# Kernel tuning notes

Measured on AMD Instinct MI355X. Metric: run time of the kernel, lower is better.

Reference implementation:

```python
import jax, jax.numpy as jnp
import numpy as np

N_NODES = 110000   # users + items per domain
NUM_USER = 60000   # item offset
ALPHA = 1.0        # gradient-reversal scale (identity in forward)


def _gcn(x, src, dst, W, b):
    # PyG GCNConv: x@W, add self-loops, symmetric D^-1/2 (A+I) D^-1/2, +bias
    xw = x @ W
    sl = jnp.arange(N_NODES)
    s = jnp.concatenate([src, sl])
    d = jnp.concatenate([dst, sl])
    deg = jax.ops.segment_sum(jnp.ones(d.shape[0], xw.dtype), d, num_segments=N_NODES)
    dinv = jnp.where(deg > 0, jax.lax.rsqrt(deg), 0.0)
    msg = xw[s] * (dinv[s] * dinv[d])[:, None]
    return jax.ops.segment_sum(msg, d, num_segments=N_NODES) + b


def _bce(p, y):
    # torch BCELoss (mean, log clamped at -100)
    lp = jnp.clip(jnp.log(p), -100.0)
    lq = jnp.clip(jnp.log(1.0 - p), -100.0)
    return -jnp.mean(y * lp + (1.0 - y) * lq)


def setup_inputs():
    key = jax.random.key(0)
    ks = jax.random.split(key, 22)
    F_IN, H, E, B = 128, 128, 1600000, 100000
    inp = {}
    inp['feats_s'] = jax.random.normal(ks[0], (N_NODES, F_IN), jnp.float32)
    inp['feats_t'] = jax.random.normal(ks[1], (N_NODES, F_IN), jnp.float32)
    inp['adj_ds'] = jax.random.randint(ks[2], (2, E), 0, N_NODES)
    inp['adj_dt'] = jax.random.randint(ks[3], (2, E), 0, N_NODES)
    inp['user_s'] = jax.random.randint(ks[4], (B,), 0, NUM_USER)
    inp['item_s'] = jax.random.randint(ks[5], (B,), 0, N_NODES - NUM_USER)
    inp['labels_s'] = jax.random.randint(ks[6], (B,), 0, 2)
    inp['user_t'] = jax.random.randint(ks[7], (B,), 0, NUM_USER)
    inp['item_t'] = jax.random.randint(ks[8], (B,), 0, N_NODES - NUM_USER)
    inp['labels_t'] = jax.random.randint(ks[9], (B,), 0, 2)
    SH = 2 * H  # sum(hidden_dims)
    inp['W1'] = jax.random.normal(ks[10], (F_IN, H), jnp.float32) / np.sqrt(F_IN)
    inp['b1'] = jnp.zeros((H,), jnp.float32)
    inp['W2'] = jax.random.normal(ks[11], (H, H), jnp.float32) / np.sqrt(H)
    inp['b2'] = jnp.zeros((H,), jnp.float32)
    inp['Wp'] = jax.random.normal(ks[12], (2 * SH, 1), jnp.float32) / np.sqrt(2 * SH)
    inp['bp'] = jnp.zeros((1,), jnp.float32)
    inp['Wdu'] = jax.random.normal(ks[13], (SH, 1), jnp.float32) / np.sqrt(SH)
    inp['bdu'] = jnp.zeros((1,), jnp.float32)
    inp['Wdi'] = jax.random.normal(ks[14], (SH, 1), jnp.float32) / np.sqrt(SH)
    inp['bdi'] = jnp.zeros((1,), jnp.float32)
    return inp


def reference(feats_s, feats_t, adj_ds, adj_dt, user_s, item_s, labels_s,
              user_t, item_t, labels_t, W1, b1, W2, b2, Wp, bp, Wdu, bdu, Wdi, bdi):
    x_ds, x_dt = feats_s, feats_t
    uf_s, if_s, uf_t, if_t = [], [], [], []
    for (W, b) in ((W1, b1), (W2, b2)):
        x_ds = jax.nn.relu(_gcn(x_ds, adj_ds[0], adj_ds[1], W, b))
        x_dt = jax.nn.relu(_gcn(x_dt, adj_dt[0], adj_dt[1], W, b))
        uf_s.append(x_ds[user_s]); if_s.append(x_ds[item_s + NUM_USER])
        uf_t.append(x_dt[user_t]); if_t.append(x_dt[item_t + NUM_USER])
    uf_s = jnp.concatenate(uf_s, axis=1); if_s = jnp.concatenate(if_s, axis=1)
    uf_t = jnp.concatenate(uf_t, axis=1); if_t = jnp.concatenate(if_t, axis=1)
    p_s = jax.nn.sigmoid(jnp.concatenate([uf_s, if_s], 1) @ Wp + bp).reshape(-1)
    p_t = jax.nn.sigmoid(jnp.concatenate([uf_t, if_t], 1) @ Wp + bp).reshape(-1)
    loss = _bce(p_s, labels_s.astype(jnp.float32)) + _bce(p_t, labels_t.astype(jnp.float32))
    # gradient reversal is identity in forward
    pu = jax.nn.sigmoid(jnp.concatenate([uf_s, uf_t], 0) @ Wdu + bdu).reshape(-1)
    pi = jax.nn.sigmoid(jnp.concatenate([if_s, if_t], 0) @ Wdi + bdi).reshape(-1)
    B = uf_s.shape[0]
    dlab = jnp.concatenate([jnp.zeros((B,), jnp.float32), jnp.ones((uf_t.shape[0],), jnp.float32)])
    domain_loss = _bce(pi, dlab) + _bce(pu, dlab)
    return loss + domain_loss * 0.1
```

## Files before the change

kernel.cpp:

```cpp
#include <hip/hip_runtime.h>

#define N_NODES 110000
#define NUM_USER 60000
#define MPAD 110080
#define ZROW N_NODES
#define BSHIFT 9
#define NBUCK 256
#define NPB 512
#define EPB 8192
#define SCAP 9216

typedef __attribute__((ext_vector_type(8))) __bf16 bf16x8;
typedef __attribute__((ext_vector_type(4))) float f32x4;
typedef __attribute__((ext_vector_type(2))) float f32x2;
typedef __attribute__((ext_vector_type(4))) unsigned int uint4v;

union UB { uint4v u; bf16x8 b; };

__device__ __forceinline__ unsigned short f2b(float f) {
    unsigned int u = __float_as_uint(f);
    unsigned int r = (u + 0x7FFFu + ((u >> 16) & 1u)) >> 16;
    return (unsigned short)r;
}
__device__ __forceinline__ float b2f(unsigned short h) {
    return __uint_as_float(((unsigned int)h) << 16);
}
__device__ __forceinline__ unsigned f2e4m3(float x) {
    unsigned u = __float_as_uint(x * 0x1p-120f);
    unsigned r = u + 0x7FFFFu + ((u >> 20) & 1u);
    return ((r >> 20) & 0x7Fu) | ((u >> 24) & 0x80u);
}
__device__ __forceinline__ float e4m3f(unsigned v) {
    unsigned bits = ((v & 0x80u) << 24) | ((v & 0x7Fu) << 20);
    return __uint_as_float(bits) * 0x1p+120f;
}


__global__ __launch_bounds__(256) void init_k(const float* __restrict__ W1, const float* __restrict__ W2,
        ushort* __restrict__ W1h, ushort* __restrict__ W1l,
        ushort* __restrict__ W2h, ushort* __restrict__ W2l,
        unsigned char* __restrict__ Tp0, unsigned char* __restrict__ Tp1,
        float* __restrict__ acc, int* __restrict__ bcnt) {
    int b = blockIdx.x, tid = threadIdx.x;
    if (b < 128) {
        const float* W = (b < 64) ? W1 : W2;
        ushort* hi = (b < 64) ? W1h : W2h;
        ushort* lo = (b < 64) ? W1l : W2l;
        int i = (b & 63) * 256 + tid;
        int k = i >> 7, n = i & 127;
        float w = W[i];
        ushort h = f2b(w);
        hi[(n << 7) | k] = h;
        lo[(n << 7) | k] = f2b(w - b2f(h));
    } else if (b < 130) {
        unsigned char* Tp = (b == 128) ? Tp0 : Tp1;
        for (int j = tid; j < (MPAD - N_NODES) * 128; j += 256)
            Tp[(size_t)N_NODES * 128 + j] = 0;
    } else {
        if (tid < 16) acc[tid] = 0.f;
        bcnt[tid] = 0;
        bcnt[256 + tid] = 0;
    }
}


__global__ __launch_bounds__(256) void bin2_k(const int* __restrict__ adj0, const int* __restrict__ adj1,
        int* __restrict__ bcnt, unsigned int* __restrict__ stg, int E, int nbE) {
    __shared__ int h[NBUCK];
    __shared__ int lcur[NBUCK];
    int b = blockIdx.x, tid = threadIdx.x;
    int dom = b / nbE, blk = b - dom * nbE;
    const int* src = (dom ? adj1 : adj0);
    const int* dst = src + E;
    unsigned int* sg = stg + (size_t)dom * NBUCK * SCAP;
    h[tid] = 0;
    __syncthreads();
    int base = blk * EPB, end = min(base + EPB, E);
    for (int i = base + tid * 4; i + 3 < end; i += 1024) {
        int4 d = *(const int4*)&dst[i];
        atomicAdd(&h[d.x >> BSHIFT], 1); atomicAdd(&h[d.y >> BSHIFT], 1);
        atomicAdd(&h[d.z >> BSHIFT], 1); atomicAdd(&h[d.w >> BSHIFT], 1);
    }
    __syncthreads();
    lcur[tid] = tid * SCAP + atomicAdd(&bcnt[dom * NBUCK + tid], h[tid]);
    __syncthreads();
    for (int i = base + tid * 4; i + 3 < end; i += 1024) {
        int4 s = *(const int4*)&src[i];
        int4 d = *(const int4*)&dst[i];
        int p;
        p = atomicAdd(&lcur[d.x >> BSHIFT], 1); sg[p] = (unsigned)s.x | ((unsigned)(d.x & (NPB - 1)) << 17);
        p = atomicAdd(&lcur[d.y >> BSHIFT], 1); sg[p] = (unsigned)s.y | ((unsigned)(d.y & (NPB - 1)) << 17);
        p = atomicAdd(&lcur[d.z >> BSHIFT], 1); sg[p] = (unsigned)s.z | ((unsigned)(d.z & (NPB - 1)) << 17);
        p = atomicAdd(&lcur[d.w >> BSHIFT], 1); sg[p] = (unsigned)s.w | ((unsigned)(d.w & (NPB - 1)) << 17);
    }
}

__global__ __launch_bounds__(256) void csr_k(const unsigned int* __restrict__ stg,
        const int* __restrict__ bcnt,
        int* __restrict__ deg, float* __restrict__ dinv, int* __restrict__ off,
        int* __restrict__ idxb, int N, int nbB) {
    __shared__ int ldeg[NPB];
    __shared__ int lcur[NPB];
    __shared__ int shp[256];
    __shared__ unsigned int lidx[SCAP];
    int b = blockIdx.x, tid = threadIdx.x;
    int dom = b / nbB, blk = b - dom * nbB;
    const unsigned int* sg = stg + ((size_t)dom * NBUCK + blk) * SCAP;
    int* degd = deg + (size_t)dom * N_NODES;
    float* dinvd = dinv + (size_t)dom * N_NODES;
    int* offd = off + (size_t)dom * N_NODES;
    int* idxd = idxb + (size_t)dom * NBUCK * SCAP;
    int node0 = blk * NPB;
    int base = blk * SCAP;
    int cnt = bcnt[dom * NBUCK + blk];
    ldeg[tid] = 0; ldeg[tid + 256] = 0;
    __syncthreads();
    for (int i = tid; i < cnt; i += 256)
        atomicAdd(&ldeg[sg[i] >> 17], 1);
    __syncthreads();
    int a0 = ldeg[2 * tid], a1 = ldeg[2 * tid + 1];
    shp[tid] = a0 + a1;
    __syncthreads();
    for (int o = 1; o < 256; o <<= 1) {
        int v = (tid >= o) ? shp[tid - o] : 0;
        __syncthreads();
        shp[tid] += v;
        __syncthreads();
    }
    int excl = shp[tid] - a0 - a1;
    lcur[2 * tid] = excl;
    lcur[2 * tid + 1] = excl + a0;
    int n0 = node0 + 2 * tid;
    if (n0 < N)     { degd[n0] = a0;     dinvd[n0] = rsqrtf(a0 + 1.f);     offd[n0] = base + excl; }
    if (n0 + 1 < N) { degd[n0 + 1] = a1; dinvd[n0 + 1] = rsqrtf(a1 + 1.f); offd[n0 + 1] = base + excl + a0; }
    __syncthreads();
    for (int i = tid; i < cnt; i += 256) {
        unsigned e = sg[i];
        int p = atomicAdd(&lcur[e >> 17], 1);
        if (p < SCAP) lidx[p] = e & 0x1FFFFu;
    }
    __syncthreads();
    for (int i = tid; i < cnt; i += 256)
        idxd[base + i] = (int)lidx[i];
}


template<bool F32A>
__global__ __launch_bounds__(256) void mm_k(const float* __restrict__ Xf0, const float* __restrict__ Xf1,
        const ushort* __restrict__ Xhi0, const ushort* __restrict__ Xhi1,
        const ushort* __restrict__ Whi, const ushort* __restrict__ Wlo,
        const float* __restrict__ dinv2, unsigned char* __restrict__ Tp0, unsigned char* __restrict__ Tp1,
        int M, int gHalf) {
    __shared__ ushort ldsW[2][1024 * 8];
    int bid = blockIdx.x;
    int dom = bid >= gHalf;
    bid -= dom * gHalf;
    const float* Xf = dom ? Xf1 : Xf0;
    const ushort* Xhi = dom ? Xhi1 : Xhi0;
    const float* dinv = dinv2 + (size_t)dom * N_NODES;
    unsigned char* Tp = dom ? Tp1 : Tp0;
    int tid = threadIdx.x;
    int wid = tid >> 6, lane = tid & 63;
    int l15 = lane & 15;
    int kg = (lane >> 4) * 8;
    int row0 = bid * 128 + wid * 32;
    int rA0 = row0 + l15;
    int rA1 = row0 + 16 + l15;
    f32x4 acc[2][8] = {};
    #pragma unroll
    for (int ph = 0; ph < 2; ph++) {
        if (ph) __syncthreads();
        #pragma unroll
        for (int i = 0; i < 8; i++) {
            int arr = i >> 2;
            int f = tid + (i & 3) * 256;
            int l = f & 63;
            int nr = ((f >> 6) & 7) * 16 + (l & 15);
            int kc = (2 * ph + (f >> 9)) * 32 + (l >> 4) * 8;
            const ushort* srcp = (arr ? Wlo : Whi) + nr * 128 + kc;
            *(uint4v*)&ldsW[arr][(size_t)f * 8] = *(const uint4v*)srcp;
        }
        __syncthreads();
        #pragma unroll
        for (int gg = 0; gg < 2; gg++) {
            int g = 2 * ph + gg;
            int k0 = g * 32 + kg;
            UB a0hi, a0lo, a1hi, a1lo;
            if (F32A) {
                #pragma unroll
                for (int s = 0; s < 2; s++) {
                    int rA = s ? rA1 : rA0;
                    float4 f0 = make_float4(0.f, 0.f, 0.f, 0.f), f1 = f0;
                    if (rA < M) {
                        f0 = *(const float4*)&Xf[(size_t)rA * 128 + k0];
                        f1 = *(const float4*)&Xf[(size_t)rA * 128 + k0 + 4];
                    }
                    float fv[8] = {f0.x, f0.y, f0.z, f0.w, f1.x, f1.y, f1.z, f1.w};
                    ushort h[8], l[8];
                    #pragma unroll
                    for (int j = 0; j < 8; j++) { h[j] = f2b(fv[j]); l[j] = f2b(fv[j] - b2f(h[j])); }
                    uint4v hu = uint4v{(uint)h[0] | ((uint)h[1] << 16), (uint)h[2] | ((uint)h[3] << 16),
                                       (uint)h[4] | ((uint)h[5] << 16), (uint)h[6] | ((uint)h[7] << 16)};
                    uint4v lu = uint4v{(uint)l[0] | ((uint)l[1] << 16), (uint)l[2] | ((uint)l[3] << 16),
                                       (uint)l[4] | ((uint)l[5] << 16), (uint)l[6] | ((uint)l[7] << 16)};
                    if (s) { a1hi.u = hu; a1lo.u = lu; } else { a0hi.u = hu; a0lo.u = lu; }
                }
            } else {
                a0hi.u = *(const uint4v*)&Xhi[(size_t)rA0 * 128 + k0];
                a1hi.u = *(const uint4v*)&Xhi[(size_t)rA1 * 128 + k0];
            }
            #pragma unroll
            for (int n = 0; n < 8; n++) {
                int fbase = ((gg * 8 + n) * 64 + lane) * 8;
                UB bhi, blo;
                bhi.u = *(const uint4v*)&ldsW[0][fbase];
                blo.u = *(const uint4v*)&ldsW[1][fbase];
                acc[0][n] = __builtin_amdgcn_mfma_f32_16x16x32_bf16(a0hi.b, bhi.b, acc[0][n], 0, 0, 0);
                acc[0][n] = __builtin_amdgcn_mfma_f32_16x16x32_bf16(a0hi.b, blo.b, acc[0][n], 0, 0, 0);
                if (F32A)
                    acc[0][n] = __builtin_amdgcn_mfma_f32_16x16x32_bf16(a0lo.b, bhi.b, acc[0][n], 0, 0, 0);
                acc[1][n] = __builtin_amdgcn_mfma_f32_16x16x32_bf16(a1hi.b, bhi.b, acc[1][n], 0, 0, 0);
                acc[1][n] = __builtin_amdgcn_mfma_f32_16x16x32_bf16(a1hi.b, blo.b, acc[1][n], 0, 0, 0);
                if (F32A)
                    acc[1][n] = __builtin_amdgcn_mfma_f32_16x16x32_bf16(a1lo.b, bhi.b, acc[1][n], 0, 0, 0);
            }
        }
    }
    #pragma unroll
    for (int s = 0; s < 2; s++) {
        int rbase = row0 + s * 16 + (lane >> 4) * 4;
        #pragma unroll
        for (int r = 0; r < 4; r++) {
            int row = rbase + r;
            if (row < M) {
                float dv = dinv[row];
                #pragma unroll
                for (int n = 0; n < 8; n++)
                    Tp[(size_t)row * 128 + n * 16 + l15] = (unsigned char)f2e4m3(dv * acc[s][n][r]);
            }
        }
    }
}


template<bool STORE_F>
__global__ __launch_bounds__(256) void aggregate_k(
        const unsigned char* __restrict__ Tp0, const unsigned char* __restrict__ Tp1,
        const int* __restrict__ idxb, const int* __restrict__ off, const int* __restrict__ deg,
        const float* __restrict__ dinv2, const float* __restrict__ bias,
        const float* __restrict__ Wp, const float* __restrict__ Wdu, const float* __restrict__ Wdi,
        int loff, float* __restrict__ nd0, float* __restrict__ nd1,
        ushort* __restrict__ ohi0, ushort* __restrict__ ohi1, int N, int gHalf) {
    int bid = blockIdx.x;
    int dom = bid >= gHalf;
    bid -= dom * gHalf;
    const unsigned char* Tp = dom ? Tp1 : Tp0;
    const int* idxd = idxb + (size_t)dom * NBUCK * SCAP;
    const int* offd = off + (size_t)dom * N_NODES;
    const int* degd = deg + (size_t)dom * N_NODES;
    const float* dinv = dinv2 + (size_t)dom * N_NODES;
    float* nd = dom ? nd1 : nd0;
    ushort* ohi = dom ? ohi1 : ohi0;

    int w = threadIdx.x >> 6, lane = threadIdx.x & 63;
    int d = bid * 4 + w;
    int grp = lane >> 4, li = lane & 15;
    int db = li * 8;
    if (d >= N) {
        if (STORE_F && grp == 0) *(uint4*)&ohi[(size_t)d * 128 + db] = make_uint4(0, 0, 0, 0);
        return;
    }
    f32x2 A0 = {0.f, 0.f}, A1 = {0.f, 0.f}, A2 = {0.f, 0.f}, A3 = {0.f, 0.f};
    int o = offd[d];
    int cnt = degd[d] + 1;
    unsigned laneoff = (unsigned)(li << 3);
    for (int c = 0; c < cnt; c += 64) {
        int p = c + lane;
        int id = ZROW;
        if (p < cnt) id = (p == 0) ? d : idxd[o + p - 1];
        int m = min(64, cnt - c);
        #pragma unroll 4
        for (int jj = 0; jj * 4 < m; jj++) {
            int s = __shfl(id, jj * 4 + grp);
            uint2 u = *(const uint2*)(Tp + (((unsigned)s << 7) | laneoff));
#if __has_builtin(__builtin_amdgcn_cvt_pk_f32_fp8)
            A0 += __builtin_amdgcn_cvt_pk_f32_fp8(u.x, false);
            A1 += __builtin_amdgcn_cvt_pk_f32_fp8(u.x, true);
            A2 += __builtin_amdgcn_cvt_pk_f32_fp8(u.y, false);
            A3 += __builtin_amdgcn_cvt_pk_f32_fp8(u.y, true);
#else
            A0 += f32x2{e4m3f(u.x & 0xFF),         e4m3f((u.x >> 8) & 0xFF)};
            A1 += f32x2{e4m3f((u.x >> 16) & 0xFF), e4m3f(u.x >> 24)};
            A2 += f32x2{e4m3f(u.y & 0xFF),         e4m3f((u.y >> 8) & 0xFF)};
            A3 += f32x2{e4m3f((u.y >> 16) & 0xFF), e4m3f(u.y >> 24)};
#endif
        }
    }
    float a0 = A0[0], a1 = A0[1], a2 = A1[0], a3 = A1[1];
    float a4 = A2[0], a5 = A2[1], a6 = A3[0], a7 = A3[1];
    #define RED2(x) { x += __shfl_xor(x, 16); x += __shfl_xor(x, 32); }
    RED2(a0) RED2(a1) RED2(a2) RED2(a3) RED2(a4) RED2(a5) RED2(a6) RED2(a7)
    #undef RED2
    float di = dinv[d];
    float4 b0 = *(const float4*)&bias[db];
    float4 b1 = *(const float4*)&bias[db + 4];
    float f0 = fmaxf(di * a0 + b0.x, 0.f);
    float f1 = fmaxf(di * a1 + b0.y, 0.f);
    float f2 = fmaxf(di * a2 + b0.z, 0.f);
    float f3 = fmaxf(di * a3 + b0.w, 0.f);
    float f4 = fmaxf(di * a4 + b1.x, 0.f);
    float f5 = fmaxf(di * a5 + b1.y, 0.f);
    float f6 = fmaxf(di * a6 + b1.z, 0.f);
    float f7 = fmaxf(di * a7 + b1.w, 0.f);
    if (STORE_F && grp == 0) {
        ushort h0 = f2b(f0), h1 = f2b(f1), h2 = f2b(f2), h3 = f2b(f3);
        ushort h4 = f2b(f4), h5 = f2b(f5), h6 = f2b(f6), h7 = f2b(f7);
        uint4 hv = make_uint4((uint)h0 | ((uint)h1 << 16), (uint)h2 | ((uint)h3 << 16),
                              (uint)h4 | ((uint)h5 << 16), (uint)h6 | ((uint)h7 << 16));
        *(uint4*)&ohi[(size_t)d * 128 + db] = hv;
    }
    const float* wsel = (grp == 0) ? Wp + loff : (grp == 1) ? Wp + 256 + loff
                      : (grp == 2) ? Wdu + loff : Wdi + loff;
    float4 w0 = *(const float4*)&wsel[db];
    float4 w1 = *(const float4*)&wsel[db + 4];
    float dt = f0 * w0.x + f1 * w0.y + f2 * w0.z + f3 * w0.w
             + f4 * w1.x + f5 * w1.y + f6 * w1.z + f7 * w1.w;
    dt += __shfl_xor(dt, 1); dt += __shfl_xor(dt, 2);
    dt += __shfl_xor(dt, 4); dt += __shfl_xor(dt, 8);
    if (li == 0) nd[(size_t)d * 4 + grp] = dt;
}


__device__ __forceinline__ float sp100(float z) {
    float sp = (z > 0.f) ? (z + log1pf(expf(-z))) : log1pf(expf(z));
    return fminf(sp, 100.f);
}
__device__ __forceinline__ float wred64(float x) {
    #pragma unroll
    for (int o = 32; o > 0; o >>= 1) x += __shfl_xor(x, o);
    return x;
}

__global__ __launch_bounds__(256) void loss_k(
        const float4* __restrict__ nd1_0, const float4* __restrict__ nd1_1,
        const float4* __restrict__ nd2_0, const float4* __restrict__ nd2_1,
        const int* __restrict__ user0, const int* __restrict__ user1,
        const int* __restrict__ item0, const int* __restrict__ item1,
        const int* __restrict__ lab0, const int* __restrict__ lab1,
        const float* __restrict__ bp, const float* __restrict__ bdu, const float* __restrict__ bdi,
        float* __restrict__ acc, int B, int gHalf) {
    __shared__ float sh[3][4];
    int bid = blockIdx.x;
    int dom = bid >= gHalf;
    bid -= dom * gHalf;
    const float4* nd1 = dom ? nd1_1 : nd1_0;
    const float4* nd2 = dom ? nd2_1 : nd2_0;
    const int* user = dom ? user1 : user0;
    const int* item = dom ? item1 : item0;
    const int* labels = dom ? lab1 : lab0;
    int gtid = bid * blockDim.x + threadIdx.x;
    int nth = gHalf * blockDim.x;
    float bpv = bp[0], bduv = bdu[0], bdiv = bdi[0];
    float lp = 0.f, lu = 0.f, li = 0.f;
    for (int s = gtid; s < B; s += nth) {
        int u = user[s];
        int it = item[s] + NUM_USER;
        float4 a = nd1[u], b = nd2[u], c = nd1[it], dd = nd2[it];
        float zp = a.x + b.x + c.y + dd.y + bpv;
        float zu = a.z + b.z + bduv;
        float zi = c.w + dd.w + bdiv;
        lp += labels[s] ? sp100(-zp) : sp100(zp);
        lu += dom ? sp100(-zu) : sp100(zu);
        li += dom ? sp100(-zi) : sp100(zi);
    }
    lp = wred64(lp); lu = wred64(lu); li = wred64(li);
    int lane = threadIdx.x & 63, w = threadIdx.x >> 6;
    if (lane == 0) { sh[0][w] = lp; sh[1][w] = lu; sh[2][w] = li; }
    __syncthreads();
    if (threadIdx.x == 0) {
        float s0 = 0.f, s1 = 0.f, s2 = 0.f;
        for (int j = 0; j < 4; j++) { s0 += sh[0][j]; s1 += sh[1][j]; s2 += sh[2][j]; }
        atomicAdd(&acc[dom], s0);
        atomicAdd(&acc[2], s1);
        atomicAdd(&acc[3], s2);
    }
}

__global__ void fin_k(const float* __restrict__ acc, float* __restrict__ out, int B) {
    float invB = 1.f / (float)B;
    out[0] = acc[0] * invB + acc[1] * invB + 0.1f * ((acc[2] + acc[3]) * (0.5f * invB));
}


extern "C" void kernel_launch(void* const* d_in, const int* in_sizes, int n_in,
                              void* d_out, int out_size, void* d_ws, size_t ws_size,
                              hipStream_t stream) {
    const float* feats[2] = {(const float*)d_in[0], (const float*)d_in[1]};
    const int* adj[2]    = {(const int*)d_in[2], (const int*)d_in[3]};
    const int* user[2]   = {(const int*)d_in[4], (const int*)d_in[7]};
    const int* item[2]   = {(const int*)d_in[5], (const int*)d_in[8]};
    const int* labels[2] = {(const int*)d_in[6], (const int*)d_in[9]};
    const float* Wl[2] = {(const float*)d_in[10], (const float*)d_in[12]};
    const float* bl[2] = {(const float*)d_in[11], (const float*)d_in[13]};
    const float* Wp  = (const float*)d_in[14];
    const float* bp  = (const float*)d_in[15];
    const float* Wdu = (const float*)d_in[16];
    const float* bdu = (const float*)d_in[17];
    const float* Wdi = (const float*)d_in[18];
    const float* bdi = (const float*)d_in[19];

    const int E = in_sizes[2] / 2;
    const int B = in_sizes[4];
    const int N = N_NODES;

    char* w = (char*)d_ws;
    unsigned char* Tp0 = (unsigned char*)w; w += (size_t)MPAD * 128;
    unsigned char* Tp1 = (unsigned char*)w; w += (size_t)MPAD * 128;
    ushort* Fhi0 = (ushort*)w; w += (size_t)MPAD * 128 * 2;
    ushort* Fhi1 = (ushort*)w; w += (size_t)MPAD * 128 * 2;
    ushort* W1h  = (ushort*)w; w += 16384 * 2;
    ushort* W1l  = (ushort*)w; w += 16384 * 2;
    ushort* W2h  = (ushort*)w; w += 16384 * 2;
    ushort* W2l  = (ushort*)w; w += 16384 * 2;
    float* nd1_0 = (float*)w; w += (size_t)MPAD * 16;
    float* nd1_1 = (float*)w; w += (size_t)MPAD * 16;
    float* nd2_0 = (float*)w; w += (size_t)MPAD * 16;
    float* nd2_1 = (float*)w; w += (size_t)MPAD * 16;
    int*   deg  = (int*)w;   w += (size_t)2 * N * 4;
    float* dinv = (float*)w; w += (size_t)2 * N * 4;
    int*   off  = (int*)w;   w += (size_t)2 * N * 4;
    int*   idxb = (int*)w;   w += (size_t)2 * NBUCK * SCAP * 4;
    unsigned int* stg = (unsigned int*)w; w += (size_t)2 * NBUCK * SCAP * 4;
    int*   bcnt = (int*)w;   w += 2 * NBUCK * 4;
    float* acc  = (float*)w; w += 64;

    int nbE = (E + EPB - 1) / EPB;
    int nbB = (N + NPB - 1) / NPB;
    int gMM = MPAD / 128;
    int gAG = MPAD / 4;

    init_k<<<131, 256, 0, stream>>>(Wl[0], Wl[1], W1h, W1l, W2h, W2l, Tp0, Tp1, acc, bcnt);

    bin2_k<<<2 * nbE, 256, 0, stream>>>(adj[0], adj[1], bcnt, stg, E, nbE);
    csr_k<<<2 * nbB, 256, 0, stream>>>(stg, bcnt, deg, dinv, off, idxb, N, nbB);

    mm_k<true><<<2 * gMM, 256, 0, stream>>>(feats[0], feats[1], nullptr, nullptr,
                                            W1h, W1l, dinv, Tp0, Tp1, N, gMM);
    aggregate_k<true><<<2 * gAG, 256, 0, stream>>>(Tp0, Tp1, idxb, off, deg, dinv, bl[0],
                                                   Wp, Wdu, Wdi, 0, nd1_0, nd1_1, Fhi0, Fhi1, N, gAG);
    mm_k<false><<<2 * gMM, 256, 0, stream>>>(nullptr, nullptr, Fhi0, Fhi1,
                                             W2h, W2l, dinv, Tp0, Tp1, N, gMM);
    aggregate_k<false><<<2 * gAG, 256, 0, stream>>>(Tp0, Tp1, idxb, off, deg, dinv, bl[1],
                                                    Wp, Wdu, Wdi, 128, nd2_0, nd2_1, nullptr, nullptr, N, gAG);

    loss_k<<<256, 256, 0, stream>>>((const float4*)nd1_0, (const float4*)nd1_1,
                                    (const float4*)nd2_0, (const float4*)nd2_1,
                                    user[0], user[1], item[0], item[1], labels[0], labels[1],
                                    bp, bdu, bdi, acc, B, 128);
    fin_k<<<1, 1, 0, stream>>>(acc, (float*)d_out, B);
}
```

Before: 406.5 us.

## Process two destination nodes per wavefront in GCN aggregation

The aggregation kernel now assigns two destination nodes per 64-lane wavefront (one per 32-lane half) instead of one, each half split into two 16-lane groups that gather alternate neighbors. Neighbor indices are loaded directly per iteration rather than staged and shuffled, and the projection dot-products compute two outputs per group. The grid is halved accordingly. This aims to cut idle lanes and loop overhead for the low average degree (~15 neighbors), but the two halves iterate to the larger of their counts, so divergence can waste work when degrees differ.

```diff
diff --git a/kernel.cpp b/kernel.cpp
--- a/kernel.cpp
+++ b/kernel.cpp
@@ -263,26 +263,31 @@
     ushort* ohi = dom ? ohi1 : ohi0;
 
     int w = threadIdx.x >> 6, lane = threadIdx.x & 63;
-    int d = bid * 4 + w;
-    int grp = lane >> 4, li = lane & 15;
+    int half = lane >> 5;
+    int grp = (lane >> 4) & 1;
+    int li = lane & 15;
+    int d = bid * 8 + w * 2 + half;
     int db = li * 8;
-    if (d >= N) {
+    bool valid = d < N;
+    int o = 0, cnt = 0;
+    if (valid) { o = offd[d]; cnt = degd[d] + 1; }
+    int cmax = max(cnt, __shfl_xor(cnt, 32));
+    if (!valid) {
         if (STORE_F && grp == 0) *(uint4*)&ohi[(size_t)d * 128 + db] = make_uint4(0, 0, 0, 0);
         return;
     }
     f32x2 A0 = {0.f, 0.f}, A1 = {0.f, 0.f}, A2 = {0.f, 0.f}, A3 = {0.f, 0.f};
-    int o = offd[d];
-    int cnt = degd[d] + 1;
     unsigned laneoff = (unsigned)(li << 3);
-    for (int c = 0; c < cnt; c += 64) {
-        int p = c + lane;
-        int id = ZROW;
-        if (p < cnt) id = (p == 0) ? d : idxd[o + p - 1];
-        int m = min(64, cnt - c);
+    int ob = o + grp - 1;
+    for (int c = 0; c < cmax; c += 32) {
+        int m = min(32, cmax - c);
         #pragma unroll 4
-        for (int jj = 0; jj * 4 < m; jj++) {
-            int s = __shfl(id, jj * 4 + grp);
-            uint2 u = *(const uint2*)(Tp + (((unsigned)s << 7) | laneoff));
+        for (int jj = 0; jj * 2 < m; jj++) {
+            int p = c + jj * 2 + grp;
+            int ia = max(ob + c + jj * 2, 0);
+            int iv = idxd[ia];
+            int id = (p == 0) ? d : ((p < cnt) ? iv : ZROW);
+            uint2 u = *(const uint2*)(Tp + (((unsigned)id << 7) | laneoff));
 #if __has_builtin(__builtin_amdgcn_cvt_pk_f32_fp8)
             A0 += __builtin_amdgcn_cvt_pk_f32_fp8(u.x, false);
             A1 += __builtin_amdgcn_cvt_pk_f32_fp8(u.x, true);
@@ -298,9 +303,9 @@
     }
     float a0 = A0[0], a1 = A0[1], a2 = A1[0], a3 = A1[1];
     float a4 = A2[0], a5 = A2[1], a6 = A3[0], a7 = A3[1];
-    #define RED2(x) { x += __shfl_xor(x, 16); x += __shfl_xor(x, 32); }
-    RED2(a0) RED2(a1) RED2(a2) RED2(a3) RED2(a4) RED2(a5) RED2(a6) RED2(a7)
-    #undef RED2
+    #define RED1(x) { x += __shfl_xor(x, 16); }
+    RED1(a0) RED1(a1) RED1(a2) RED1(a3) RED1(a4) RED1(a5) RED1(a6) RED1(a7)
+    #undef RED1
     float di = dinv[d];
     float4 b0 = *(const float4*)&bias[db];
     float4 b1 = *(const float4*)&bias[db + 4];
@@ -319,15 +324,21 @@
                               (uint)h4 | ((uint)h5 << 16), (uint)h6 | ((uint)h7 << 16));
         *(uint4*)&ohi[(size_t)d * 128 + db] = hv;
     }
-    const float* wsel = (grp == 0) ? Wp + loff : (grp == 1) ? Wp + 256 + loff
-                      : (grp == 2) ? Wdu + loff : Wdi + loff;
-    float4 w0 = *(const float4*)&wsel[db];
-    float4 w1 = *(const float4*)&wsel[db + 4];
-    float dt = f0 * w0.x + f1 * w0.y + f2 * w0.z + f3 * w0.w
-             + f4 * w1.x + f5 * w1.y + f6 * w1.z + f7 * w1.w;
-    dt += __shfl_xor(dt, 1); dt += __shfl_xor(dt, 2);
-    dt += __shfl_xor(dt, 4); dt += __shfl_xor(dt, 8);
-    if (li == 0) nd[(size_t)d * 4 + grp] = dt;
+    const float* ws0 = grp ? Wdu + loff : Wp + loff;
+    const float* ws1 = grp ? Wdi + loff : Wp + 256 + loff;
+    float4 w00 = *(const float4*)&ws0[db];
+    float4 w01 = *(const float4*)&ws0[db + 4];
+    float4 w10 = *(const float4*)&ws1[db];
+    float4 w11 = *(const float4*)&ws1[db + 4];
+    float dt0 = f0 * w00.x + f1 * w00.y + f2 * w00.z + f3 * w00.w
+              + f4 * w01.x + f5 * w01.y + f6 * w01.z + f7 * w01.w;
+    float dt1 = f0 * w10.x + f1 * w10.y + f2 * w10.z + f3 * w10.w
+              + f4 * w11.x + f5 * w11.y + f6 * w11.z + f7 * w11.w;
+    dt0 += __shfl_xor(dt0, 1); dt1 += __shfl_xor(dt1, 1);
+    dt0 += __shfl_xor(dt0, 2); dt1 += __shfl_xor(dt1, 2);
+    dt0 += __shfl_xor(dt0, 4); dt1 += __shfl_xor(dt1, 4);
+    dt0 += __shfl_xor(dt0, 8); dt1 += __shfl_xor(dt1, 8);
+    if (li == 0) *(float2*)&nd[(size_t)d * 4 + grp * 2] = make_float2(dt0, dt1);
 }
 
 
@@ -437,7 +448,7 @@
     int nbE = (E + EPB - 1) / EPB;
     int nbB = (N + NPB - 1) / NPB;
     int gMM = MPAD / 128;
-    int gAG = MPAD / 4;
+    int gAG = MPAD / 8;
 
     init_k<<<131, 256, 0, stream>>>(Wl[0], Wl[1], W1h, W1l, W2h, W2l, Tp0, Tp1, acc, bcnt);
 
```

After: 335.0 us. 17.6% less time.
